# Optimization experiments

Measured on AMD Instinct MI355X. Metric: run time of the kernel, lower is better.

The kernel has to match this reference:

```python
import jax, jax.numpy as jnp
import numpy as np

B, SQ, SK, D, M = 4, 2048, 2048, 512, 8  # Sq must equal Sk (see notes)


def setup_inputs() -> dict:
    key = jax.random.key(0)
    ks = jax.random.split(key, 6)
    return {
        "Q": jax.random.normal(ks[0], (B, SQ, D), jnp.float32),
        "K": jax.random.normal(ks[1], (B, SK, D), jnp.float32),
        "V": jax.random.normal(ks[2], (B, SK, D), jnp.float32),  # unused by the module's math (overwritten by K')
        "miu": 0.02 * jax.random.normal(ks[3], (M, D), jnp.float32),          # cluster centers
        "Wq": jax.random.normal(ks[4], (M, D, D), jnp.float32) / np.sqrt(D),  # per-cluster Q expert weights (in,out)
        "bq": jnp.zeros((M, D), jnp.float32),
        "Wk": jax.random.normal(ks[5], (M, D, D), jnp.float32) / np.sqrt(D),  # per-cluster K expert weights
        "bk": jnp.zeros((M, D), jnp.float32),
    }


def reference(Q, K, V, miu, Wq, bq, Wk, bk):
    Bq, Sq, d = Q.shape
    Sk = K.shape[1]
    scale = 1.0 / (d ** 0.5)

    # --- hard routing: argmax over dot-product scores to cluster centers ---
    x = jnp.concatenate([Q, K], axis=1)                      # (B, Sq+Sk, d)
    route = jnp.einsum('btd,md->btm', x, miu) * scale        # (B, Sq+Sk, M)
    assign = jnp.argmax(route, axis=-1)                      # (B, Sq+Sk)
    aq, ak = assign[:, :Sq], assign[:, Sq:]                  # query / key cluster ids

    # --- per-cluster expert MLP (Linear -> GELU(exact); Dropout is eval identity) ---
    # compute all M experts, then gather the routed one per token
    yq = jax.nn.gelu(jnp.einsum('bsd,mde->bsme', Q, Wq) + bq, approximate=False)  # (B,Sq,M,d)
    Qp = jnp.take_along_axis(yq, aq[:, :, None, None], axis=2)[:, :, 0, :]        # (B,Sq,d)
    yk = jax.nn.gelu(jnp.einsum('bsd,mde->bsme', K, Wk) + bk, approximate=False)  # (B,Sk,M,d)
    Kp = jnp.take_along_axis(yk, ak[:, :, None, None], axis=2)[:, :, 0, :]        # (B,Sk,d)
    Vp = Kp  # module sets V = K_prime

    # --- clustered attention: query attends only to keys in its own cluster ---
    logits = jnp.einsum('bqd,bkd->bqk', Qp, Kp) * scale      # (B,Sq,Sk)
    mask = aq[:, :, None] == ak[:, None, :]                  # (B,Sq,Sk)
    neg = jnp.finfo(logits.dtype).min
    w = jax.nn.softmax(jnp.where(mask, logits, neg), axis=-1)
    O = jnp.einsum('bqk,bkd->bqd', w, Vp)                    # (B,Sq,d)

    # fallback: queries whose cluster has no keys in this batch -> mean of V'
    has_key = mask.any(axis=-1)                              # (B,Sq)
    O = jnp.where(has_key[..., None], O, Vp.mean(axis=1)[:, None, :])

    return O + Q
```

## Files before the change

kernel.cpp:

```cpp
#include <hip/hip_runtime.h>
#include <hip/hip_bf16.h>
#include <math.h>

#define BB  4
#define SQL 2048
#define SKL 2048
#define DD  512
#define MM  8
#define NG  (BB*MM)
#define NTOK (BB*(SQL+SKL))
#define PCAP (8u*1024u*1024u)
#define KTCAP ((size_t)DD*11264)
#define UCAP  (34u*1024u*1024u)
#define PROJCAP 512
#define SCCAP   6144
#define PVCAP   512
#define SCALE 0.04419417382415922f

typedef __attribute__((ext_vector_type(8))) short short8v;
typedef __attribute__((ext_vector_type(4))) float f32x4;

__device__ __forceinline__ ushort f2b(float x) {
    union { __hip_bfloat16 h; ushort u; } cv; cv.h = __float2bfloat16(x); return cv.u;
}
__device__ __forceinline__ float b2f(ushort x) {
    union { ushort u; __hip_bfloat16 h; } cv; cv.u = x; return __bfloat162float(cv.h);
}
__device__ __forceinline__ float gelu_fast(float x) {
    float z2 = 1.5957691216057308f * x * (1.0f + 0.044715f * x * x);
    float e = __expf(fminf(z2, 40.0f));
    return x * e * __builtin_amdgcn_rcpf(e + 1.0f);
}
__device__ __forceinline__ void gload16(const ushort* g, ushort* l) {
    __builtin_amdgcn_global_load_lds(
        (const __attribute__((address_space(1))) void*)g,
        (__attribute__((address_space(3))) void*)l, 16, 0, 0);
}

__global__ void k_route(const float* __restrict__ Q, const float* __restrict__ K,
                        const float* __restrict__ miu,
                        int* __restrict__ aq, int* __restrict__ ak,
                        ushort* __restrict__ Qb16, ushort* __restrict__ Kb16) {
    int g    = blockIdx.x * 4 + (threadIdx.x >> 6);
    int lane = threadIdx.x & 63;
    int b = g >> 12;
    int t = g & 4095;
    bool isQ = (t < SQL);
    size_t rowoff = isQ ? (size_t)(b*SQL + t) * DD : (size_t)(b*SKL + (t - SQL)) * DD;
    const float* x = (isQ ? Q : K) + rowoff;
    ushort* yb = (isQ ? Qb16 : Kb16) + rowoff;
    double acc[MM];
#pragma unroll
    for (int m = 0; m < MM; ++m) acc[m] = 0.0;
#pragma unroll
    for (int j = 0; j < 8; ++j) {
        int i = j * 64 + lane;
        float xv = x[i];
        yb[i] = f2b(xv);
#pragma unroll
        for (int m = 0; m < MM; ++m) acc[m] += (double)xv * (double)miu[m*DD + i];
    }
#pragma unroll
    for (int m = 0; m < MM; ++m) {
#pragma unroll
        for (int off = 32; off > 0; off >>= 1)
            acc[m] += __shfl_down(acc[m], off);
    }
    if (lane == 0) {
        double best = acc[0]; int bi = 0;
#pragma unroll
        for (int m = 1; m < MM; ++m) if (acc[m] > best) { best = acc[m]; bi = m; }
        if (isQ) aq[b*SQL + t] = bi; else ak[b*SKL + (t - SQL)] = bi;
    }
}

__global__ void k_compact(const int* __restrict__ aq, const int* __restrict__ ak,
                          int* __restrict__ qcnt, int* __restrict__ kcnt,
                          int* __restrict__ qlist, int* __restrict__ klist) {
    int idx = blockIdx.x;
    int isK = idx >> 5;
    int g   = idx & 31;
    int b = g >> 3, m = g & 7;
    const int* a = isK ? (ak + b*SKL) : (aq + b*SQL);
    int* list = (isK ? klist : qlist) + g*SQL;
    int lane = threadIdx.x;
    int base = 0;
    for (int c = 0; c < SQL; c += 64) {
        int s = c + lane;
        bool f = (a[s] == m);
        unsigned long long mk = __ballot(f);
        int before = __popcll(mk & ((1ull << lane) - 1ull));
        if (f) list[base + before] = s;
        base += __popcll(mk);
    }
    if (lane == 0) (isK ? kcnt : qcnt)[g] = base;
}

__global__ void k_soff(const int* __restrict__ qcnt, const int* __restrict__ kcnt,
                       int* __restrict__ soff, int* __restrict__ pboff,
                       int* __restrict__ qoff, int* __restrict__ koff,
                       int* __restrict__ tkoff, int* __restrict__ counts,
                       int* __restrict__ projl, int* __restrict__ scl,
                       int* __restrict__ pvl) {
    __shared__ int pbase[64], sbase[32], pvbase[32];
    int lane = threadIdx.x;
    if (lane == 0) {
        int sacc = 0, pacc = 0, qa = 0, ka = 0, ta = 0;
        for (int g = 0; g < NG; ++g) {
            soff[g] = sacc; pboff[g] = pacc; qoff[g] = qa; koff[g] = ka; tkoff[g] = ta;
            int nq = qcnt[g], nk = kcnt[g];
            int nks = ((nk + 63) & ~63) + 32;
            sacc += nq * nk; pacc += nq * nks; qa += nq; ka += nk; ta += DD * nks;
        }
        soff[NG] = sacc; pboff[NG] = pacc; qoff[NG] = qa; koff[NG] = ka; tkoff[NG] = ta;
        int pj = 0, sc = 0, pv = 0;
        for (int sg = 0; sg < 64; ++sg) {
            int n = (sg >= 32 ? kcnt : qcnt)[sg & 31];
            pbase[sg] = pj; pj += (n + 127) >> 7;
        }
        for (int g = 0; g < NG; ++g) {
            int nq = qcnt[g], nk = kcnt[g];
            sbase[g] = sc; pvbase[g] = pv;
            if (nq > 0 && nk > 0) {
                sc += ((nq + 63) >> 6) * ((nk + 63) >> 6);
                pv += (nq + 31) >> 5;
            }
        }
        counts[0] = pj; counts[1] = sc; counts[2] = pv;
    }
    __syncthreads();
    {
        int sg = lane;
        int side = sg >> 5, g = sg & 31;
        int n = (side ? kcnt : qcnt)[g];
        int ntile = (n + 127) >> 7;
        int base = pbase[sg];
        for (int ty = 0; ty < ntile; ++ty)
            projl[base + ty] = (side << 11) | (g << 6) | ty;
    }
    if (lane < 32) {
        int g = lane;
        int nq = qcnt[g], nk = kcnt[g];
        if (nq > 0 && nk > 0) {
            int nqt = (nq + 63) >> 6, nkt = (nk + 63) >> 6;
            int idx = sbase[g];
            for (int qy = 0; qy < nqt; ++qy)
                for (int ky = 0; ky < nkt; ++ky)
                    scl[idx++] = (g << 10) | (qy << 5) | ky;
            int nqt32 = (nq + 31) >> 5;
            int pidx = pvbase[g];
            for (int qy = 0; qy < nqt32; ++qy)
                pvl[pidx++] = (g << 7) | qy;
        }
    }
}

__global__ void k_cvtW(const float* __restrict__ Wq, const float* __restrict__ Wk,
                       ushort* __restrict__ Wqt, ushort* __restrict__ Wkt) {
    __shared__ float tile[32][33];
    int mm = blockIdx.x; int isK = mm >> 3; int m = mm & 7;
    const float* W = (isK ? Wk : Wq) + (size_t)m * DD * DD;
    ushort* Wt = (isK ? Wkt : Wqt) + (size_t)m * DD * DD;
    int d0 = blockIdx.y * 32, e0 = blockIdx.z * 32;
    int tx = threadIdx.x, ty = threadIdx.y;
    for (int i = ty; i < 32; i += 8)
        tile[i][tx] = W[(size_t)(d0 + i) * DD + e0 + tx];
    __syncthreads();
    for (int i = ty; i < 32; i += 8)
        Wt[(size_t)(e0 + i) * DD + d0 + tx] = f2b(tile[tx][i]);
}

__global__ __launch_bounds__(256) void k_proj_mfma(
        const ushort* __restrict__ Qb16, const ushort* __restrict__ Kb16,
        const ushort* __restrict__ Wqt, const ushort* __restrict__ Wkt,
        const float* __restrict__ bq, const float* __restrict__ bk,
        const int* __restrict__ qcnt, const int* __restrict__ kcnt,
        const int* __restrict__ qlist, const int* __restrict__ klist,
        const int* __restrict__ qoff, const int* __restrict__ koff,
        const int* __restrict__ tkoff, const int* __restrict__ counts,
        const int* __restrict__ projl,
        ushort* __restrict__ Qc, ushort* __restrict__ Kc, ushort* __restrict__ KcT) {
    __shared__ ushort lds[2][16384];
    __shared__ int rows[128];
    int tid = threadIdx.x;
    int wid = tid >> 6, lane = tid & 63;
    int wr = wid >> 1, wc = wid & 1;
    int lr = lane & 15;
    int h = lane >> 4;
    int x7 = lr & 7;
    int csz0 = ((h ^ x7) << 3);
    int csz1 = (((4 | h) ^ x7) << 3);
    int c0 = blockIdx.y * 128;
    int e8 = lane >> 3;
    int glcs = (((lane & 7) ^ e8) << 3);
    int cnt = counts[0];
    int vbid = (blockIdx.x & 7) * 24 + (blockIdx.x >> 3);

    for (int slot = vbid; slot < cnt; slot += gridDim.x) {
        int e = projl[slot];
        int isK = (e >> 11) & 1, g = (e >> 6) & 31, ty = e & 63;
        int n = (isK ? kcnt : qcnt)[g];
        int obase = (isK ? koff : qoff)[g];
        int b = g >> 3, m = g & 7;
        const ushort* Xtok = (isK ? Kb16 : Qb16) + (size_t)b * SQL * DD;
        const ushort* Wt = (isK ? Wkt : Wqt) + (size_t)m * DD * DD;
        const float* bias = (isK ? bk : bq) + m * DD;
        const int* list = (isK ? klist : qlist) + g * SQL;
        int t0 = ty * 128;

        __syncthreads();
        if (tid < 128) rows[tid] = list[min(t0 + tid, n - 1)];
        __syncthreads();

        auto STAGE = [&](int buf, int kt) {
            int d0 = kt * 64;
            ushort* As = lds[buf];
            ushort* Bs = lds[buf] + 8192;
#pragma unroll
            for (int j0 = 0; j0 < 4; ++j0) {
                int j = wid + j0 * 4;
                int rtok = rows[j*8 + e8];
                gload16(Xtok + (size_t)rtok * DD + d0 + glcs, As + j*512);
                int rB = c0 + j*8 + e8;
                gload16(Wt + (size_t)rB * DD + d0 + glcs, Bs + j*512);
            }
        };

        f32x4 acc[4][4];
#pragma unroll
        for (int t = 0; t < 4; ++t)
#pragma unroll
            for (int c = 0; c < 4; ++c) acc[t][c] = (f32x4){0.f, 0.f, 0.f, 0.f};

        STAGE(0, 0);
        __syncthreads();
        for (int kt = 0; kt < 8; ++kt) {
            int cur = kt & 1;
            if (kt < 7) STAGE(cur ^ 1, kt + 1);
            const ushort* As = lds[cur];
            const ushort* Bs = lds[cur] + 8192;
#pragma unroll
            for (int kk = 0; kk < 2; ++kk) {
                int csz = kk ? csz1 : csz0;
                short8v a[4], bb[4];
#pragma unroll
                for (int t = 0; t < 4; ++t)
                    a[t] = *(const short8v*)(As + (wr*64 + t*16 + lr)*64 + csz);
#pragma unroll
                for (int c = 0; c < 4; ++c)
                    bb[c] = *(const short8v*)(Bs + (wc*64 + c*16 + lr)*64 + csz);
#pragma unroll
                for (int t = 0; t < 4; ++t)
#pragma unroll
                    for (int c = 0; c < 4; ++c)
                        acc[t][c] = __builtin_amdgcn_mfma_f32_16x16x32_bf16(a[t], bb[c], acc[t][c], 0, 0, 0);
            }
            __syncthreads();
        }

        float bcache[4];
#pragma unroll
        for (int c = 0; c < 4; ++c) bcache[c] = bias[c0 + wc*64 + c*16 + lr];

        int rb = (lane >> 4) << 2;
        int nk2 = kcnt[g];
        int nks = ((nk2 + 63) & ~63) + 32;
        int tk = tkoff[g];
        ushort* Yc = isK ? Kc : Qc;
#pragma unroll
        for (int t = 0; t < 4; ++t) {
            int grow = ty*128 + wr*64 + t*16 + rb;
#pragma unroll
            for (int c = 0; c < 4; ++c) {
                int col = c0 + wc*64 + c*16 + lr;
                float v[4];
#pragma unroll
                for (int r = 0; r < 4; ++r) v[r] = gelu_fast(acc[t][c][r] + bcache[c]);
                if (!isK) {
#pragma unroll
                    for (int r = 0; r < 4; ++r)
                        if (grow + r < n)
                            Yc[(size_t)(obase + grow + r) * DD + col] = f2b(v[r] * SCALE);
                } else {
#pragma unroll
                    for (int r = 0; r < 4; ++r)
                        if (grow + r < n)
                            Yc[(size_t)(obase + grow + r) * DD + col] = f2b(v[r]);
                    size_t taddr = (size_t)tk + (size_t)col * nks + grow;
                    if (grow + 3 < n) {
                        ushort4 o; o.x = f2b(v[0]); o.y = f2b(v[1]); o.z = f2b(v[2]); o.w = f2b(v[3]);
                        *(ushort4*)(KcT + taddr) = o;
                    } else {
#pragma unroll
                        for (int r = 0; r < 4; ++r)
                            if (grow + r < n) KcT[taddr + r] = f2b(v[r]);
                    }
                }
            }
        }
    }
}

__global__ void k_meanpart(const ushort* __restrict__ Kc, const int* __restrict__ koff,
                           float* __restrict__ part) {
    int b = blockIdx.x, ch = blockIdx.y;
    int d = threadIdx.x;
    int base = koff[b*8] + ch * 64;
    float a0 = 0.f, a1 = 0.f;
    for (int t = 0; t < 64; ++t) {
        const ushort* row = Kc + (size_t)(base + t) * DD;
        a0 += b2f(row[d]); a1 += b2f(row[d + 256]);
    }
    part[((size_t)(b*32 + ch))*DD + d]       = a0;
    part[((size_t)(b*32 + ch))*DD + d + 256] = a1;
}
__global__ void k_meanfinal(const float* __restrict__ part, float* __restrict__ meanV) {
    int b = blockIdx.x; int d = threadIdx.x;
    float a0 = 0.f;
    for (int ch = 0; ch < 32; ++ch)
        a0 += part[((size_t)(b*32 + ch))*DD + d];
    meanV[b*DD + d] = a0 * (1.0f/SKL);
}

__global__ __launch_bounds__(256) void k_scores_mfma(
        const ushort* __restrict__ Qc, const ushort* __restrict__ Kc,
        const int* __restrict__ qcnt, const int* __restrict__ kcnt,
        const int* __restrict__ qoff, const int* __restrict__ koff,
        const int* __restrict__ soff, const int* __restrict__ counts,
        const int* __restrict__ scl, float* __restrict__ S) {
    int tid = threadIdx.x, wid = tid >> 6, lane = tid & 63;
    int wr = wid >> 1, wc = wid & 1;
    int lr = lane & 15, lk = (lane >> 4) * 8;
    int cnt = counts[1];
    int vbid = (blockIdx.x & 7) * 128 + (blockIdx.x >> 3);
    for (int slot = vbid; slot < cnt; slot += gridDim.x) {
        int e = scl[slot];
        int g = (e >> 10) & 31, qt = ((e >> 5) & 31) * 64, kt = (e & 31) * 64;
        int nq = qcnt[g], nk = kcnt[g];
        int qb = qoff[g], kb = koff[g];

        const ushort* ap[2];
#pragma unroll
        for (int t = 0; t < 2; ++t)
            ap[t] = Qc + (size_t)(qb + min(qt + wr*32 + t*16 + lr, nq - 1)) * DD + lk;
        const ushort* bp[2];
#pragma unroll
        for (int c = 0; c < 2; ++c)
            bp[c] = Kc + (size_t)(kb + min(kt + wc*32 + c*16 + lr, nk - 1)) * DD + lk;

        f32x4 acc[2][2];
#pragma unroll
        for (int t = 0; t < 2; ++t)
#pragma unroll
            for (int c = 0; c < 2; ++c) acc[t][c] = (f32x4){0.f, 0.f, 0.f, 0.f};

        short8v a[2], bb[2], an[2], bn[2];
#pragma unroll
        for (int t = 0; t < 2; ++t) a[t]  = *(const short8v*)(ap[t]);
#pragma unroll
        for (int c = 0; c < 2; ++c) bb[c] = *(const short8v*)(bp[c]);
        for (int d0 = 0; d0 < DD; d0 += 32) {
            int dn = d0 + 32;
            if (dn < DD) {
#pragma unroll
                for (int t = 0; t < 2; ++t) an[t] = *(const short8v*)(ap[t] + dn);
#pragma unroll
                for (int c = 0; c < 2; ++c) bn[c] = *(const short8v*)(bp[c] + dn);
            }
#pragma unroll
            for (int t = 0; t < 2; ++t)
#pragma unroll
                for (int c = 0; c < 2; ++c)
                    acc[t][c] = __builtin_amdgcn_mfma_f32_16x16x32_bf16(a[t], bb[c], acc[t][c], 0, 0, 0);
#pragma unroll
            for (int t = 0; t < 2; ++t) a[t] = an[t];
#pragma unroll
            for (int c = 0; c < 2; ++c) bb[c] = bn[c];
        }

        int sbase = soff[g];
        int rb = (lane >> 4) << 2;
#pragma unroll
        for (int t = 0; t < 2; ++t) {
#pragma unroll
            for (int r = 0; r < 4; ++r) {
                int gr = qt + wr*32 + t*16 + rb + r;
                if (gr >= nq) continue;
#pragma unroll
                for (int c = 0; c < 2; ++c) {
                    int gc = kt + wc*32 + c*16 + lr;
                    if (gc < nk) S[(size_t)sbase + (size_t)gr*nk + gc] = acc[t][c][r];
                }
            }
        }
    }
}

__global__ void k_softmax(const int* __restrict__ qcnt, const int* __restrict__ kcnt,
                          const int* __restrict__ soff, const int* __restrict__ pboff,
                          float* __restrict__ S, ushort* __restrict__ Pb) {
    int g = blockIdx.x;
    int nq = qcnt[g], nk = kcnt[g];
    if (nk == 0) return;
    int wid = threadIdx.x >> 6, lane = threadIdx.x & 63;
    int nk64 = (nk + 63) & ~63;
    int nks = nk64 + 32;
    for (int row = blockIdx.y * 16 + wid; row < nq; row += 512) {
        float* p = S + (size_t)soff[g] + (size_t)row * nk;
        ushort* pr = Pb + (size_t)pboff[g] + (size_t)row * nks;
        float mx = -3.4e38f;
        for (int c = lane; c < nk; c += 64) mx = fmaxf(mx, p[c]);
#pragma unroll
        for (int off = 32; off > 0; off >>= 1) mx = fmaxf(mx, __shfl_xor(mx, off));
        float sm = 0.f;
        for (int c = lane; c < nk; c += 64) { float e = __expf(p[c] - mx); p[c] = e; sm += e; }
#pragma unroll
        for (int off = 32; off > 0; off >>= 1) sm += __shfl_xor(sm, off);
        float inv = 1.0f / sm;
        for (int c = lane; c < nk64; c += 64) {
            float v = (c < nk) ? p[c] * inv : 0.f;
            pr[c] = f2b(v);
        }
    }
}

__global__ __launch_bounds__(256) void k_pv_mfma(
        const ushort* __restrict__ Pb, const ushort* __restrict__ KcT,
        const float* __restrict__ Q,
        const int* __restrict__ qcnt, const int* __restrict__ kcnt,
        const int* __restrict__ tkoff, const int* __restrict__ pboff,
        const int* __restrict__ qlist, const int* __restrict__ counts,
        const int* __restrict__ pvl, float* __restrict__ out) {
    __shared__ ushort plds[2][2048];
    __shared__ ushort klds[2][8192];
    int tid = threadIdx.x, wid = tid >> 6, lane = tid & 63;
    int lr = lane & 15;
    int h  = lane >> 4;
    int x7 = lr & 7;
    int csz0 = ((h ^ x7) << 3);
    int csz1 = (((4 | h) ^ x7) << 3);
    int e8 = lane >> 3;
    int glcs = (((lane & 7) ^ e8) << 3);
    int cnt = counts[2];
    int vbid = (blockIdx.x & 7) * 32 + (blockIdx.x >> 3);
    int dt = blockIdx.y * 128;

    for (int slot = vbid; slot < cnt; slot += gridDim.x) {
        int e = pvl[slot];
        int g = e >> 7, qt = (e & 127) * 32;
        int nq = qcnt[g], nk = kcnt[g];
        int b = g >> 3;
        int nk64 = (nk + 63) & ~63;
        int nks = nk64 + 32;
        int tk = tkoff[g], pbase = pboff[g];

        const ushort* psrc = Pb + (size_t)pbase
            + (size_t)min(qt + wid*8 + e8, nq - 1) * nks + glcs;
        const ushort* ksrc[4];
#pragma unroll
        for (int p = 0; p < 4; ++p) {
            int col = (wid + p*4) * 8 + e8;
            ksrc[p] = KcT + (size_t)tk + (size_t)(dt + col) * nks + glcs;
        }

        auto STAGE = [&](int buf, int kt) {
            int k0 = kt * 64;
            gload16(psrc + k0, &plds[buf][wid * 512]);
#pragma unroll
            for (int p = 0; p < 4; ++p)
                gload16(ksrc[p] + k0, &klds[buf][(wid + p*4) * 512]);
        };

        f32x4 acc[2][2];
#pragma unroll
        for (int t = 0; t < 2; ++t)
#pragma unroll
            for (int c = 0; c < 2; ++c) acc[t][c] = (f32x4){0.f, 0.f, 0.f, 0.f};

        int nt = nk64 >> 6;
        __syncthreads();
        STAGE(0, 0);
        __syncthreads();
        for (int kt = 0; kt < nt; ++kt) {
            int cur = kt & 1;
            if (kt + 1 < nt) STAGE(cur ^ 1, kt + 1);
            const ushort* P_ = plds[cur];
            const ushort* K_ = klds[cur];
#pragma unroll
            for (int kk = 0; kk < 2; ++kk) {
                int csz = kk ? csz1 : csz0;
                short8v a[2], bb[2];
#pragma unroll
                for (int t = 0; t < 2; ++t)
                    a[t] = *(const short8v*)(P_ + (t*16 + lr)*64 + csz);
#pragma unroll
                for (int c = 0; c < 2; ++c)
                    bb[c] = *(const short8v*)(K_ + (wid*32 + c*16 + lr)*64 + csz);
#pragma unroll
                for (int t = 0; t < 2; ++t)
#pragma unroll
                    for (int c = 0; c < 2; ++c)
                        acc[t][c] = __builtin_amdgcn_mfma_f32_16x16x32_bf16(a[t], bb[c], acc[t][c], 0, 0, 0);
            }
            __syncthreads();
        }

        int rb = (lane >> 4) << 2;
#pragma unroll
        for (int t = 0; t < 2; ++t) {
#pragma unroll
            for (int r = 0; r < 4; ++r) {
                int gr = qt + t*16 + rb + r;
                if (gr >= nq) continue;
                int qrow = qlist[g*SQL + gr];
                size_t obase = ((size_t)(b*SQL) + qrow) * DD;
#pragma unroll
                for (int c = 0; c < 2; ++c) {
                    size_t o = obase + dt + wid*32 + c*16 + lr;
                    out[o] = acc[t][c][r] + Q[o];
                }
            }
        }
    }
}

__global__ void k_fallback(const float* __restrict__ Q, const float* __restrict__ meanV,
                           const int* __restrict__ qcnt, const int* __restrict__ kcnt,
                           const int* __restrict__ qlist, float* __restrict__ out) {
    int g = blockIdx.x;
    if (kcnt[g] != 0) return;
    int nq = qcnt[g]; int b = g >> 3;
    int r0 = blockIdx.y * 256;
    int rend = min(r0 + 256, nq);
    for (int r = r0; r < rend; ++r) {
        int qrow = qlist[g*SQL + r];
        size_t base = ((size_t)(b*SQL) + qrow) * DD;
        for (int d = threadIdx.x; d < DD; d += 256)
            out[base + d] = meanV[b*DD + d] + Q[base + d];
    }
}

extern "C" void kernel_launch(void* const* d_in, const int* in_sizes, int n_in,
                              void* d_out, int out_size, void* d_ws, size_t ws_size,
                              hipStream_t stream) {
    (void)in_sizes; (void)n_in; (void)out_size; (void)ws_size;
    const float* Q   = (const float*)d_in[0];
    const float* K   = (const float*)d_in[1];
    const float* miu = (const float*)d_in[3];
    const float* Wq  = (const float*)d_in[4];
    const float* bq  = (const float*)d_in[5];
    const float* Wk  = (const float*)d_in[6];
    const float* bk  = (const float*)d_in[7];
    float* out = (float*)d_out;
    char* ws = (char*)d_ws;

    size_t off = 0;
    auto alloc = [&](size_t bytes) { size_t o = off; off += (bytes + 255) & ~(size_t)255; return o; };
    int*   aq     = (int*)  (ws + alloc((size_t)BB*SQL*4));
    int*   ak     = (int*)  (ws + alloc((size_t)BB*SKL*4));
    int*   qcnt   = (int*)  (ws + alloc(NG*4));
    int*   kcnt   = (int*)  (ws + alloc(NG*4));
    int*   soff   = (int*)  (ws + alloc((NG+1)*4));
    int*   pboff  = (int*)  (ws + alloc((NG+1)*4));
    int*   qoff   = (int*)  (ws + alloc((NG+1)*4));
    int*   koff   = (int*)  (ws + alloc((NG+1)*4));
    int*   tkoff  = (int*)  (ws + alloc((NG+1)*4));
    int*   counts = (int*)  (ws + alloc(16*4));
    int*   projl  = (int*)  (ws + alloc(PROJCAP*4));
    int*   scl    = (int*)  (ws + alloc(SCCAP*4));
    int*   pvl    = (int*)  (ws + alloc(PVCAP*4));
    int*   qlist  = (int*)  (ws + alloc((size_t)NG*SQL*4));
    int*   klist  = (int*)  (ws + alloc((size_t)NG*SKL*4));
    float* part   = (float*)(ws + alloc((size_t)BB*32*DD*4));
    float* meanV  = (float*)(ws + alloc((size_t)BB*DD*4));
    ushort* Qc    = (ushort*)(ws + alloc((size_t)BB*SQL*DD*2));
    ushort* Kc    = (ushort*)(ws + alloc((size_t)BB*SKL*DD*2));
    ushort* KcT   = (ushort*)(ws + alloc(KTCAP*2));
    ushort* Pb    = (ushort*)(ws + alloc((size_t)PCAP*2));
    size_t uoff = alloc((size_t)UCAP);
    float* S     = (float*)(ws + uoff);
    ushort* Wqt  = (ushort*)(ws + uoff);
    ushort* Wkt  = Wqt  + (size_t)MM*DD*DD;
    ushort* Qb16 = Wkt  + (size_t)MM*DD*DD;
    ushort* Kb16 = Qb16 + (size_t)BB*SQL*DD;

    k_route     <<<NTOK/4, 256, 0, stream>>>(Q, K, miu, aq, ak, Qb16, Kb16);
    k_compact   <<<NG*2, 64, 0, stream>>>(aq, ak, qcnt, kcnt, qlist, klist);
    k_soff      <<<1, 64, 0, stream>>>(qcnt, kcnt, soff, pboff, qoff, koff, tkoff,
                                       counts, projl, scl, pvl);
    k_cvtW      <<<dim3(16, 16, 16), dim3(32, 8), 0, stream>>>(Wq, Wk, Wqt, Wkt);
    k_proj_mfma <<<dim3(192, 4), 256, 0, stream>>>(Qb16, Kb16, Wqt, Wkt, bq, bk,
                                                   qcnt, kcnt, qlist, klist, qoff, koff,
                                                   tkoff, counts, projl, Qc, Kc, KcT);
    k_meanpart  <<<dim3(BB, 32), 256, 0, stream>>>(Kc, koff, part);
    k_meanfinal <<<BB, 512, 0, stream>>>(part, meanV);
    k_scores_mfma<<<1024, 256, 0, stream>>>(Qc, Kc, qcnt, kcnt, qoff, koff, soff,
                                            counts, scl, S);
    k_softmax   <<<dim3(NG, 32), 1024, 0, stream>>>(qcnt, kcnt, soff, pboff, S, Pb);
    k_pv_mfma   <<<dim3(256, 4), 256, 0, stream>>>(Pb, KcT, Q, qcnt, kcnt, tkoff, pboff,
                                                   qlist, counts, pvl, out);
    k_fallback  <<<dim3(NG, 8), 256, 0, stream>>>(Q, meanV, qcnt, kcnt, qlist, out);
}
```

Baseline: 164.0 us.

## Stage Q/K tiles through double-buffered swizzled LDS in scores MFMA kernel

The scores kernel now cooperatively loads 64x64 bf16 tiles of Q and K into double-buffered shared memory with an XOR swizzle, using a gload16 helper. MFMA fragments are then read from LDS instead of each wave issuing redundant direct global loads. This cuts duplicate global traffic between waves that share rows and overlaps the next tile load with compute. In exchange it adds barriers per K-step and uses 32KB of LDS per block, which may lower occupancy.

```diff
diff --git a/kernel.cpp b/kernel.cpp
--- a/kernel.cpp
+++ b/kernel.cpp
@@ -328,9 +328,16 @@
         const int* __restrict__ qoff, const int* __restrict__ koff,
         const int* __restrict__ soff, const int* __restrict__ counts,
         const int* __restrict__ scl, float* __restrict__ S) {
+    __shared__ ushort lds[2][8192];
     int tid = threadIdx.x, wid = tid >> 6, lane = tid & 63;
     int wr = wid >> 1, wc = wid & 1;
-    int lr = lane & 15, lk = (lane >> 4) * 8;
+    int lr = lane & 15;
+    int h  = lane >> 4;
+    int x7 = lr & 7;
+    int csz0 = ((h ^ x7) << 3);
+    int csz1 = (((4 | h) ^ x7) << 3);
+    int e8 = lane >> 3;
+    int glcs = (((lane & 7) ^ e8) << 3);
     int cnt = counts[1];
     int vbid = (blockIdx.x & 7) * 128 + (blockIdx.x >> 3);
     for (int slot = vbid; slot < cnt; slot += gridDim.x) {
@@ -339,43 +346,55 @@
         int nq = qcnt[g], nk = kcnt[g];
         int qb = qoff[g], kb = koff[g];
 
-        const ushort* ap[2];
+        auto STAGE = [&](int buf, int dstep) {
+            int d0 = dstep * 64;
+            ushort* As = lds[buf];
+            ushort* Bs = lds[buf] + 4096;
+#pragma unroll
+            for (int j0 = 0; j0 < 4; ++j0) {
+                int j = wid + j0 * 4;
+                if (j < 8) {
+                    int r = qb + min(qt + j*8 + e8, nq - 1);
+                    gload16(Qc + (size_t)r * DD + d0 + glcs, As + j*512);
+                } else {
+                    int jb = j - 8;
+                    int r = kb + min(kt + jb*8 + e8, nk - 1);
+                    gload16(Kc + (size_t)r * DD + d0 + glcs, Bs + jb*512);
+                }
+            }
+        };
+
+        f32x4 acc[2][2];
 #pragma unroll
         for (int t = 0; t < 2; ++t)
-            ap[t] = Qc + (size_t)(qb + min(qt + wr*32 + t*16 + lr, nq - 1)) * DD + lk;
-        const ushort* bp[2];
-#pragma unroll
-        for (int c = 0; c < 2; ++c)
-            bp[c] = Kc + (size_t)(kb + min(kt + wc*32 + c*16 + lr, nk - 1)) * DD + lk;
-
-        f32x4 acc[2][2];
-#pragma unroll
-        for (int t = 0; t < 2; ++t)
 #pragma unroll
             for (int c = 0; c < 2; ++c) acc[t][c] = (f32x4){0.f, 0.f, 0.f, 0.f};
 
-        short8v a[2], bb[2], an[2], bn[2];
-#pragma unroll
-        for (int t = 0; t < 2; ++t) a[t]  = *(const short8v*)(ap[t]);
-#pragma unroll
-        for (int c = 0; c < 2; ++c) bb[c] = *(const short8v*)(bp[c]);
-        for (int d0 = 0; d0 < DD; d0 += 32) {
-            int dn = d0 + 32;
-            if (dn < DD) {
-#pragma unroll
-                for (int t = 0; t < 2; ++t) an[t] = *(const short8v*)(ap[t] + dn);
-#pragma unroll
-                for (int c = 0; c < 2; ++c) bn[c] = *(const short8v*)(bp[c] + dn);
-            }
-#pragma unroll
-            for (int t = 0; t < 2; ++t)
+        __syncthreads();
+        STAGE(0, 0);
+        __syncthreads();
+        for (int ds = 0; ds < 8; ++ds) {
+            int cur = ds & 1;
+            if (ds < 7) STAGE(cur ^ 1, ds + 1);
+            const ushort* As = lds[cur];
+            const ushort* Bs = lds[cur] + 4096;
+#pragma unroll
+            for (int kk = 0; kk < 2; ++kk) {
+                int csz = kk ? csz1 : csz0;
+                short8v a[2], bb[2];
+#pragma unroll
+                for (int t = 0; t < 2; ++t)
+                    a[t] = *(const short8v*)(As + (wr*32 + t*16 + lr)*64 + csz);
 #pragma unroll
                 for (int c = 0; c < 2; ++c)
-                    acc[t][c] = __builtin_amdgcn_mfma_f32_16x16x32_bf16(a[t], bb[c], acc[t][c], 0, 0, 0);
-#pragma unroll
-            for (int t = 0; t < 2; ++t) a[t] = an[t];
-#pragma unroll
-            for (int c = 0; c < 2; ++c) bb[c] = bn[c];
+                    bb[c] = *(const short8v*)(Bs + (wc*32 + c*16 + lr)*64 + csz);
+#pragma unroll
+                for (int t = 0; t < 2; ++t)
+#pragma unroll
+                    for (int c = 0; c < 2; ++c)
+                        acc[t][c] = __builtin_amdgcn_mfma_f32_16x16x32_bf16(a[t], bb[c], acc[t][c], 0, 0, 0);
+            }
+            __syncthreads();
         }
 
         int sbase = soff[g];
```

New measurement: 142.4 us. 1.15x faster.
